# Optimization experiments

Measured on AMD Instinct MI355X. Metric: run time of the kernel, lower is better.

Reference implementation:

```python
import jax, jax.numpy as jnp
import numpy as np

N, E, F, H, C, G = 100000, 1600000, 128, 4, 32, 64
D = H * C  # 128, per-layer node dim
NEG_SLOPE = 0.2
BN_EPS = 1e-5


def setup_inputs() -> dict:
    key = jax.random.key(0)
    ks = jax.random.split(key, 24)
    inp = {
        "x": jax.random.normal(ks[0], (N, F), jnp.float32),
        "edge_index": jax.random.randint(ks[1], (2, E), 0, N, jnp.int64),
        "batch": jnp.sort(jax.random.randint(ks[2], (N,), 0, G, jnp.int64)),
        # GATConv layer 0: in=F, out=C per head
        "w0": jax.random.normal(ks[3], (F, H * C), jnp.float32) * 0.1,
        "att_src0": jax.random.normal(ks[4], (H, C), jnp.float32) * 0.1,
        "att_dst0": jax.random.normal(ks[5], (H, C), jnp.float32) * 0.1,
        "bias0": jax.random.normal(ks[6], (H * C,), jnp.float32) * 0.1,
        # GATConv layer 1: in=D, out=C per head
        "w1": jax.random.normal(ks[7], (D, H * C), jnp.float32) * 0.1,
        "att_src1": jax.random.normal(ks[8], (H, C), jnp.float32) * 0.1,
        "att_dst1": jax.random.normal(ks[9], (H, C), jnp.float32) * 0.1,
        "bias1": jax.random.normal(ks[10], (H * C,), jnp.float32) * 0.1,
        # BatchNorm (eval mode: running stats)
        "bn_g0": jax.random.normal(ks[11], (D,), jnp.float32) * 0.1 + 1.0,
        "bn_b0": jax.random.normal(ks[12], (D,), jnp.float32) * 0.1,
        "bn_m0": jax.random.normal(ks[13], (D,), jnp.float32) * 0.1,
        "bn_v0": jax.random.uniform(ks[14], (D,), jnp.float32) + 0.5,
        "bn_g1": jax.random.normal(ks[15], (D,), jnp.float32) * 0.1 + 1.0,
        "bn_b1": jax.random.normal(ks[16], (D,), jnp.float32) * 0.1,
        "bn_m1": jax.random.normal(ks[17], (D,), jnp.float32) * 0.1,
        "bn_v1": jax.random.uniform(ks[18], (D,), jnp.float32) + 0.5,
        # head MLP
        "lin1_w": jax.random.normal(ks[19], (D, D // 2), jnp.float32) * 0.1,
        "lin1_b": jax.random.normal(ks[20], (D // 2,), jnp.float32) * 0.1,
        "lin2_w": jax.random.normal(ks[21], (D // 2, 1), jnp.float32) * 0.1,
        "lin2_b": jax.random.normal(ks[22], (1,), jnp.float32) * 0.1,
    }
    return inp


def gat_conv(x, src, dst, w, att_s, att_d, bias):
    """PyG GATConv (concat=True, add_self_loops already in src/dst), eval mode."""
    n = x.shape[0]
    h = (x @ w).reshape(n, H, C)                       # [N,H,C]
    a_s = jnp.sum(h * att_s, axis=-1)                   # [N,H]
    a_d = jnp.sum(h * att_d, axis=-1)                   # [N,H]
    e = jax.nn.leaky_relu(a_s[src] + a_d[dst], NEG_SLOPE)  # [Etot,H]
    m = jax.ops.segment_max(e, dst, num_segments=n)
    m = jax.lax.stop_gradient(jnp.where(jnp.isfinite(m), m, 0.0))
    ex = jnp.exp(e - m[dst])
    denom = jax.ops.segment_sum(ex, dst, num_segments=n)
    alpha = ex / (denom[dst] + 1e-16)                    # segment softmax over dst
    out = jax.ops.segment_sum(h[src] * alpha[:, :, None], dst, num_segments=n)
    return out.reshape(n, H * C) + bias


def bn_eval(x, g, b, m, v):
    return (x - m) * jax.lax.rsqrt(v + BN_EPS) * g + b


def reference(x, edge_index, batch,
              w0, att_src0, att_dst0, bias0,
              w1, att_src1, att_dst1, bias1,
              bn_g0, bn_b0, bn_m0, bn_v0,
              bn_g1, bn_b1, bn_m1, bn_v1,
              lin1_w, lin1_b, lin2_w, lin2_b):
    n = x.shape[0]
    loops = jnp.arange(n, dtype=edge_index.dtype)
    src = jnp.concatenate([edge_index[0], loops])
    dst = jnp.concatenate([edge_index[1], loops])

    h = gat_conv(x, src, dst, w0, att_src0, att_dst0, bias0)
    h = jax.nn.relu(bn_eval(h, bn_g0, bn_b0, bn_m0, bn_v0))
    h = gat_conv(h, src, dst, w1, att_src1, att_dst1, bias1)
    h = jax.nn.relu(bn_eval(h, bn_g1, bn_b1, bn_m1, bn_v1))

    # global mean pool over graphs
    summed = jax.ops.segment_sum(h, batch, num_segments=G)           # [G,D]
    counts = jax.ops.segment_sum(jnp.ones((n,), h.dtype), batch, num_segments=G)
    pooled = summed / jnp.maximum(counts, 1.0)[:, None]

    z = jax.nn.relu(pooled @ lin1_w + lin1_b)
    return z @ lin2_w + lin2_b                                        # [G,1]
```

## Files before the change

### kernel.cpp

```cpp
#include <hip/hip_runtime.h>

#define GG 64
#define STRIDE 10240
#define NBINMAX 256

typedef __attribute__((ext_vector_type(8))) short short8;
typedef __attribute__((ext_vector_type(4))) float f32x4;


__device__ inline unsigned short bf16rne(float f) {
  unsigned int x = __float_as_uint(f);
  unsigned int r = (x + 0x7FFFu + ((x >> 16) & 1u)) >> 16;
  return (unsigned short)r;
}
__device__ inline unsigned int pack2(float a, float b) {
  return (unsigned int)bf16rne(a) | ((unsigned int)bf16rne(b) << 16);
}
__device__ inline float blo(unsigned int v) { return __uint_as_float(v << 16); }
__device__ inline float bhi(unsigned int v) { return __uint_as_float(v & 0xFFFF0000u); }


__global__ __launch_bounds__(256) void wprep(const float* __restrict__ w0,
                                             const float* __restrict__ w1,
                                             unsigned short* __restrict__ wt,
                                             int* __restrict__ gcur) {
  if (blockIdx.x == 0) gcur[threadIdx.x] = threadIdx.x * STRIDE;
  int idx = blockIdx.x * 256 + threadIdx.x;
  int layer = idx >> 14;
  int e = idx & 16383;
  int k = e >> 7, n = e & 127;
  float v = (layer ? w1 : w0)[e];
  unsigned short hi = bf16rne(v);
  float hif = __uint_as_float((unsigned int)hi << 16);
  unsigned short lo = bf16rne(v - hif);
  unsigned short* basep = wt + layer * 32768;
  basep[n * 128 + k] = hi;
  basep[16384 + n * 128 + k] = lo;
}


__global__ __launch_bounds__(512) void mega1(
    const float* __restrict__ in, const unsigned short* __restrict__ wtL,
    const float* __restrict__ att_s, const float* __restrict__ att_d,
    unsigned int* __restrict__ h16, float* __restrict__ a_s, float* __restrict__ a_d,
    const int* __restrict__ ei, int* __restrict__ gcur, unsigned int* __restrict__ pairs,
    const int* __restrict__ batch, int* __restrict__ gstart,
    int N, int E, int bG, int P1B) {
  __shared__ unsigned short xh[128][40], xl[128][40];
  __shared__ int hist[NBINMAX], gbase[NBINMAX], lcur[NBINMAX];
  int bid = blockIdx.x;
  int t = threadIdx.x;

  if (bid < bG) {
    int base = bid * 128;
    int lane = t & 63, w = t >> 6;
    int l15 = lane & 15, lg = lane >> 4;
    int hd = w & 3;
    int n0 = hd * 32;
    int rh = w >> 2;

    f32x4 zero4 = {0.f, 0.f, 0.f, 0.f};
    f32x4 acc[4][2];
    #pragma unroll
    for (int rt = 0; rt < 4; ++rt) { acc[rt][0] = zero4; acc[rt][1] = zero4; }

    int sr = t >> 2;
    int sc = (t & 3) * 8;
    int gr = base + sr;
    int rc = gr < N ? gr : (N - 1);
    const float* xpf = in + (size_t)rc * 128 + sc;

    const unsigned short* wh0 = &wtL[(size_t)(n0 + l15) * 128];
    const unsigned short* wh1 = &wtL[(size_t)(n0 + 16 + l15) * 128];

    float4 u0 = *(const float4*)(xpf + 0);
    float4 u1 = *(const float4*)(xpf + 4);
    short8 cbh0 = *(const short8*)(wh0 + lg * 8);
    short8 cbh1 = *(const short8*)(wh1 + lg * 8);
    short8 cbl0 = *(const short8*)(wh0 + 16384 + lg * 8);
    short8 cbl1 = *(const short8*)(wh1 + 16384 + lg * 8);

    #pragma unroll
    for (int kt = 0; kt < 4; ++kt) {
      if (kt) __syncthreads();
      {
        unsigned int b0 = __float_as_uint(u0.x), b1 = __float_as_uint(u0.y);
        unsigned int b2 = __float_as_uint(u0.z), b3 = __float_as_uint(u0.w);
        unsigned int b4 = __float_as_uint(u1.x), b5 = __float_as_uint(u1.y);
        unsigned int b6 = __float_as_uint(u1.z), b7 = __float_as_uint(u1.w);
        *(unsigned int*)&xh[sr][sc + 0] = __builtin_amdgcn_perm(b1, b0, 0x07060302u);
        *(unsigned int*)&xh[sr][sc + 2] = __builtin_amdgcn_perm(b3, b2, 0x07060302u);
        *(unsigned int*)&xh[sr][sc + 4] = __builtin_amdgcn_perm(b5, b4, 0x07060302u);
        *(unsigned int*)&xh[sr][sc + 6] = __builtin_amdgcn_perm(b7, b6, 0x07060302u);
        float r0 = u0.x - __uint_as_float(b0 & 0xFFFF0000u);
        float r1 = u0.y - __uint_as_float(b1 & 0xFFFF0000u);
        float r2 = u0.z - __uint_as_float(b2 & 0xFFFF0000u);
        float r3 = u0.w - __uint_as_float(b3 & 0xFFFF0000u);
        float r4 = u1.x - __uint_as_float(b4 & 0xFFFF0000u);
        float r5 = u1.y - __uint_as_float(b5 & 0xFFFF0000u);
        float r6 = u1.z - __uint_as_float(b6 & 0xFFFF0000u);
        float r7 = u1.w - __uint_as_float(b7 & 0xFFFF0000u);
        *(unsigned int*)&xl[sr][sc + 0] =
            __builtin_amdgcn_perm(__float_as_uint(r1), __float_as_uint(r0), 0x07060302u);
        *(unsigned int*)&xl[sr][sc + 2] =
            __builtin_amdgcn_perm(__float_as_uint(r3), __float_as_uint(r2), 0x07060302u);
        *(unsigned int*)&xl[sr][sc + 4] =
            __builtin_amdgcn_perm(__float_as_uint(r5), __float_as_uint(r4), 0x07060302u);
        *(unsigned int*)&xl[sr][sc + 6] =
            __builtin_amdgcn_perm(__float_as_uint(r7), __float_as_uint(r6), 0x07060302u);
      }
      __syncthreads();
      float4 v0 = u0, v1 = u1;
      short8 nbh0 = cbh0, nbh1 = cbh1, nbl0 = cbl0, nbl1 = cbl1;
      if (kt < 3) {
        int k1 = (kt + 1) * 32;
        v0 = *(const float4*)(xpf + k1);
        v1 = *(const float4*)(xpf + k1 + 4);
        nbh0 = *(const short8*)(wh0 + k1 + lg * 8);
        nbh1 = *(const short8*)(wh1 + k1 + lg * 8);
        nbl0 = *(const short8*)(wh0 + 16384 + k1 + lg * 8);
        nbl1 = *(const short8*)(wh1 + 16384 + k1 + lg * 8);
      }
      #pragma unroll
      for (int rt = 0; rt < 4; ++rt) {
        int row = rh * 64 + rt * 16 + l15;
        short8 fah = *(const short8*)&xh[row][lg * 8];
        short8 fal = *(const short8*)&xl[row][lg * 8];
        acc[rt][0] = __builtin_amdgcn_mfma_f32_16x16x32_bf16(fah, cbh0, acc[rt][0], 0, 0, 0);
        acc[rt][1] = __builtin_amdgcn_mfma_f32_16x16x32_bf16(fah, cbh1, acc[rt][1], 0, 0, 0);
        acc[rt][0] = __builtin_amdgcn_mfma_f32_16x16x32_bf16(fal, cbh0, acc[rt][0], 0, 0, 0);
        acc[rt][1] = __builtin_amdgcn_mfma_f32_16x16x32_bf16(fal, cbh1, acc[rt][1], 0, 0, 0);
        acc[rt][0] = __builtin_amdgcn_mfma_f32_16x16x32_bf16(fah, cbl0, acc[rt][0], 0, 0, 0);
        acc[rt][1] = __builtin_amdgcn_mfma_f32_16x16x32_bf16(fah, cbl1, acc[rt][1], 0, 0, 0);
      }
      u0 = v0; u1 = v1;
      cbh0 = nbh0; cbh1 = nbh1; cbl0 = nbl0; cbl1 = nbl1;
    }

    int headg = hd;
    float as0 = att_s[n0 + l15], as1 = att_s[n0 + 16 + l15];
    float ad0 = att_d[n0 + l15], ad1 = att_d[n0 + 16 + l15];
    #pragma unroll
    for (int rt = 0; rt < 4; ++rt) {
      float ps[4], pd[4];
      #pragma unroll
      for (int q = 0; q < 4; ++q) {
        float c0v = acc[rt][0][q], c1v = acc[rt][1][q];
        float pp0 = __shfl_xor(c0v, 1), pp1 = __shfl_xor(c1v, 1);
        int row = base + rh * 64 + rt * 16 + lg * 4 + q;
        if (!(l15 & 1) && row < N) {
          h16[(size_t)row * 64 + (n0 + l15) / 2]      = pack2(c0v, pp0);
          h16[(size_t)row * 64 + (n0 + 16 + l15) / 2] = pack2(c1v, pp1);
        }
        ps[q] = c0v * as0 + c1v * as1;
        pd[q] = c0v * ad0 + c1v * ad1;
      }
      #pragma unroll
      for (int m = 1; m <= 8; m <<= 1) {
        #pragma unroll
        for (int q = 0; q < 4; ++q) { ps[q] += __shfl_xor(ps[q], m); pd[q] += __shfl_xor(pd[q], m); }
      }
      if (l15 == 0) {
        #pragma unroll
        for (int q = 0; q < 4; ++q) {
          int row = base + rh * 64 + rt * 16 + lg * 4 + q;
          if (row < N) { a_s[row * 4 + headg] = ps[q]; a_d[row * 4 + headg] = pd[q]; }
        }
      }
    }
  } else if (bid < bG + P1B) {
    int tot = E + N;
    int base = (bid - bG) * 4096;
    if (t < NBINMAX) hist[t] = 0;
    __syncthreads();
    int sarr[8], darr[8];
    #pragma unroll
    for (int k = 0; k < 8; ++k) {
      int i = base + k * 512 + t;
      if (i < tot) {
        int s, d;
        if (i < E) { s = ei[i]; d = ei[E + i]; } else { s = i - E; d = s; }
        sarr[k] = s; darr[k] = d;
        atomicAdd(&hist[d >> 9], 1);
      } else darr[k] = -1;
    }
    __syncthreads();
    if (t < NBINMAX) {
      int c = hist[t];
      gbase[t] = (c > 0) ? atomicAdd(&gcur[t], c) : 0;
      lcur[t] = 0;
    }
    __syncthreads();
    #pragma unroll
    for (int k = 0; k < 8; ++k) {
      int d = darr[k];
      if (d >= 0) {
        int b = d >> 9;
        int p = gbase[b] + atomicAdd(&lcur[b], 1);
        pairs[p] = ((unsigned int)(d & 511) << 17) | (unsigned int)sarr[k];
      }
    }
  } else {
    int i = (bid - bG - P1B) * 512 + t;
    if (i < N) {
      int g = batch[i];
      if (i == 0 || batch[i - 1] != g) gstart[g] = i;
    }
  }
}


__global__ __launch_bounds__(256) void mega2(
    const unsigned int* __restrict__ pairs, const int* __restrict__ gcur,
    int* __restrict__ ssrc, int* __restrict__ offsets, int* __restrict__ counts,
    const int* __restrict__ gstart, int* __restrict__ go, int* __restrict__ ge,
    int N, int NBIN) {
  __shared__ int ncnt[512], ncur[512], excl_s[512];
  __shared__ int wsum[4];
  int b = blockIdx.x;
  int t = threadIdx.x;
  if (b < NBIN) {
    int pb = b * STRIDE;
    int cnt = gcur[b] - pb;
    ncnt[t] = 0; ncnt[t + 256] = 0;
    __syncthreads();
    for (int e = t; e < cnt; e += 256) {
      unsigned int v = pairs[pb + e];
      atomicAdd(&ncnt[v >> 17], 1);
    }
    __syncthreads();
    int c0 = ncnt[2 * t], c1 = ncnt[2 * t + 1];
    int ps = c0 + c1;
    int lane = t & 63, w = t >> 6;
    int x = ps;
    #pragma unroll
    for (int s = 1; s < 64; s <<= 1) { int y = __shfl_up(x, s); if (lane >= s) x += y; }
    if (lane == 63) wsum[w] = x;
    __syncthreads();
    int woff = 0;
    for (int i = 0; i < w; ++i) woff += wsum[i];
    int ep = woff + x - ps;
    excl_s[2 * t]     = ep;
    excl_s[2 * t + 1] = ep + c0;
    __syncthreads();
    int binstart = b << 9;
    for (int i = t; i < 512; i += 256) {
      ncur[i] = excl_s[i];
      int node = binstart + i;
      if (node < N) { offsets[node] = pb + excl_s[i]; counts[node] = ncnt[i]; }
    }
    __syncthreads();
    for (int e = t; e < cnt; e += 256) {
      unsigned int v = pairs[pb + e];
      int dl = v >> 17;
      int p = atomicAdd(&ncur[dl], 1);
      ssrc[pb + p] = (int)(v & 0x1FFFF);
    }
  } else if (t < 64) {
    int g = t;
    int s = gstart[g];
    int v = (s < 0) ? 0x7FFFFFFF : s;
    int suf = v;
    #pragma unroll
    for (int off = 1; off < 64; off <<= 1) {
      int x = __shfl_down(suf, off);
      if (g + off < 64) suf = min(suf, x);
    }
    int nxt = __shfl_down(suf, 1);
    if (g == 63) nxt = 0x7FFFFFFF;
    int e = nxt == 0x7FFFFFFF ? N : nxt;
    if (s < 0) { go[g] = e; ge[g] = e; }
    else       { go[g] = s; ge[g] = e; }
  }
}


__global__ __launch_bounds__(512) void gemm_bf16(
    const unsigned int* __restrict__ in, const unsigned short* __restrict__ wtL,
    const float* __restrict__ att_s, const float* __restrict__ att_d,
    unsigned int* __restrict__ h16, float* __restrict__ a_s,
    float* __restrict__ a_d, int N) {
  __shared__ unsigned short xh[128][40];
  int t = threadIdx.x;
  int base = blockIdx.x * 128;
  int lane = t & 63, w = t >> 6;
  int l15 = lane & 15, lg = lane >> 4;
  int hd = w & 3;
  int n0 = hd * 32;
  int rh = w >> 2;

  f32x4 zero4 = {0.f, 0.f, 0.f, 0.f};
  f32x4 acc[4][2];
  #pragma unroll
  for (int rt = 0; rt < 4; ++rt) { acc[rt][0] = zero4; acc[rt][1] = zero4; }

  int sr = t >> 2;
  int sc = (t & 3) * 8;
  int gr = base + sr;
  int rc = gr < N ? gr : (N - 1);
  const unsigned int* xpb = in + (size_t)rc * 64 + (sc >> 1);

  const unsigned short* wh0 = &wtL[(size_t)(n0 + l15) * 128];
  const unsigned short* wh1 = &wtL[(size_t)(n0 + 16 + l15) * 128];

  uint4 p0 = *(const uint4*)(xpb + 0);
  short8 cbh0 = *(const short8*)(wh0 + lg * 8);
  short8 cbh1 = *(const short8*)(wh1 + lg * 8);
  short8 cbl0 = *(const short8*)(wh0 + 16384 + lg * 8);
  short8 cbl1 = *(const short8*)(wh1 + 16384 + lg * 8);

  #pragma unroll
  for (int kt = 0; kt < 4; ++kt) {
    if (kt) __syncthreads();
    *(uint4*)&xh[sr][sc] = p0;
    __syncthreads();
    uint4 q0 = p0;
    short8 nbh0 = cbh0, nbh1 = cbh1, nbl0 = cbl0, nbl1 = cbl1;
    if (kt < 3) {
      int k1 = (kt + 1) * 32;
      q0 = *(const uint4*)(xpb + (k1 >> 1));
      nbh0 = *(const short8*)(wh0 + k1 + lg * 8);
      nbh1 = *(const short8*)(wh1 + k1 + lg * 8);
      nbl0 = *(const short8*)(wh0 + 16384 + k1 + lg * 8);
      nbl1 = *(const short8*)(wh1 + 16384 + k1 + lg * 8);
    }
    #pragma unroll
    for (int rt = 0; rt < 4; ++rt) {
      int row = rh * 64 + rt * 16 + l15;
      short8 fah = *(const short8*)&xh[row][lg * 8];
      acc[rt][0] = __builtin_amdgcn_mfma_f32_16x16x32_bf16(fah, cbh0, acc[rt][0], 0, 0, 0);
      acc[rt][1] = __builtin_amdgcn_mfma_f32_16x16x32_bf16(fah, cbh1, acc[rt][1], 0, 0, 0);
      acc[rt][0] = __builtin_amdgcn_mfma_f32_16x16x32_bf16(fah, cbl0, acc[rt][0], 0, 0, 0);
      acc[rt][1] = __builtin_amdgcn_mfma_f32_16x16x32_bf16(fah, cbl1, acc[rt][1], 0, 0, 0);
    }
    p0 = q0;
    cbh0 = nbh0; cbh1 = nbh1; cbl0 = nbl0; cbl1 = nbl1;
  }

  int headg = hd;
  float as0 = att_s[n0 + l15], as1 = att_s[n0 + 16 + l15];
  float ad0 = att_d[n0 + l15], ad1 = att_d[n0 + 16 + l15];
  #pragma unroll
  for (int rt = 0; rt < 4; ++rt) {
    float ps[4], pd[4];
    #pragma unroll
    for (int q = 0; q < 4; ++q) {
      float c0v = acc[rt][0][q], c1v = acc[rt][1][q];
      float pp0 = __shfl_xor(c0v, 1), pp1 = __shfl_xor(c1v, 1);
      int row = base + rh * 64 + rt * 16 + lg * 4 + q;
      if (!(l15 & 1) && row < N) {
        h16[(size_t)row * 64 + (n0 + l15) / 2]      = pack2(c0v, pp0);
        h16[(size_t)row * 64 + (n0 + 16 + l15) / 2] = pack2(c1v, pp1);
      }
      ps[q] = c0v * as0 + c1v * as1;
      pd[q] = c0v * ad0 + c1v * ad1;
    }
    #pragma unroll
    for (int m = 1; m <= 8; m <<= 1) {
      #pragma unroll
      for (int q = 0; q < 4; ++q) { ps[q] += __shfl_xor(ps[q], m); pd[q] += __shfl_xor(pd[q], m); }
    }
    if (l15 == 0) {
      #pragma unroll
      for (int q = 0; q < 4; ++q) {
        int row = base + rh * 64 + rt * 16 + lg * 4 + q;
        if (row < N) { a_s[row * 4 + headg] = ps[q]; a_d[row * 4 + headg] = pd[q]; }
      }
    }
  }
}


#define ACCP(EX, V0, V1)                                                       \
  { float2 ex2 = make_float2(EX, EX);                                          \
    acc2[0] += ex2 * make_float2(blo(V0.x), bhi(V0.x));                        \
    acc2[1] += ex2 * make_float2(blo(V0.y), bhi(V0.y));                        \
    acc2[2] += ex2 * make_float2(blo(V0.z), bhi(V0.z));                        \
    acc2[3] += ex2 * make_float2(blo(V0.w), bhi(V0.w));                        \
    acc2[4] += ex2 * make_float2(blo(V1.x), bhi(V1.x));                        \
    acc2[5] += ex2 * make_float2(blo(V1.y), bhi(V1.y));                        \
    acc2[6] += ex2 * make_float2(blo(V1.z), bhi(V1.z));                        \
    acc2[7] += ex2 * make_float2(blo(V1.w), bhi(V1.w)); }

__global__ __launch_bounds__(256) void gat_aggregate(
    const unsigned int* __restrict__ h16, const float* __restrict__ a_s, const float* __restrict__ a_d,
    const int* __restrict__ offsets, const int* __restrict__ counts, const int* __restrict__ ssrc,
    const float* __restrict__ bias,
    const float* __restrict__ bn_g, const float* __restrict__ bn_b,
    const float* __restrict__ bn_m, const float* __restrict__ bn_v,
    unsigned int* __restrict__ y16, int N) {
  __shared__ float part[4][8][132];
  int wv = threadIdx.x >> 6;
  int lane = threadIdx.x & 63;
  int wid = blockIdx.x * 4 + wv;
  if (wid >= N) return;
  int off = offsets[wid], cnt = counts[wid];
  int eg = lane >> 3;
  int j  = lane & 7;
  int hh = j >> 1;
  float ad = a_d[wid * 4 + hh];

  float2 acc2[8] = {};
  float den = 0.f;

  int sA = ssrc[off + (eg < cnt ? eg : 0)];
  int iB0 = eg + 8;
  int sB = ssrc[off + (iB0 < cnt ? iB0 : 0)];
  float asA = a_s[sA * 4 + hh];
  float asB = a_s[sB * 4 + hh];

  for (int i = eg; i < cnt; i += 16) {
    const uint4* hpA = (const uint4*)(h16 + (size_t)sA * 64 + j * 8);
    uint4 va0 = hpA[0], va1 = hpA[1];
    const uint4* hpB = (const uint4*)(h16 + (size_t)sB * 64 + j * 8);
    uint4 vb0 = hpB[0], vb1 = hpB[1];
    int in0 = i + 16, in1 = i + 24;
    int snA = ssrc[off + (in0 < cnt ? in0 : 0)];
    int snB = ssrc[off + (in1 < cnt ? in1 : 0)];
    float anA = a_s[snA * 4 + hh];
    float anB = a_s[snB * 4 + hh];
    float eA = asA + ad; eA = eA > 0.f ? eA : 0.2f * eA;
    float exA = __expf(eA);
    float eB = asB + ad; eB = eB > 0.f ? eB : 0.2f * eB;
    float exB = ((i + 8) < cnt) ? __expf(eB) : 0.f;
    den += exA + exB;
    ACCP(exA, va0, va1)
    ACCP(exB, vb0, vb1)
    sA = snA; sB = snB; asA = anA; asB = anB;
  }

  den += __shfl_xor(den, 8);
  den += __shfl_xor(den, 16);
  den += __shfl_xor(den, 32);
  den = __shfl(den, (lane >> 4) * 2);

  float* pw = &part[wv][eg][j * 16];
  *(float4*)(pw + 0)  = make_float4(acc2[0].x, acc2[0].y, acc2[1].x, acc2[1].y);
  *(float4*)(pw + 4)  = make_float4(acc2[2].x, acc2[2].y, acc2[3].x, acc2[3].y);
  *(float4*)(pw + 8)  = make_float4(acc2[4].x, acc2[4].y, acc2[5].x, acc2[5].y);
  *(float4*)(pw + 12) = make_float4(acc2[6].x, acc2[6].y, acc2[7].x, acc2[7].y);
  asm volatile("s_waitcnt lgkmcnt(0)" ::: "memory");

  int d = lane * 2;
  float r0 = 0.f, r1 = 0.f;
  #pragma unroll
  for (int g = 0; g < 8; ++g) {
    float2 v = *(const float2*)(&part[wv][g][d]);
    r0 += v.x; r1 += v.y;
  }

  float inv = 1.f / (den + 1e-16f);
  float2 bi = *(const float2*)(&bias[d]);
  float2 g2 = *(const float2*)(&bn_g[d]);
  float2 b2 = *(const float2*)(&bn_b[d]);
  float2 m2 = *(const float2*)(&bn_m[d]);
  float2 v2 = *(const float2*)(&bn_v[d]);
  float o0 = r0 * inv + bi.x;
  float o1 = r1 * inv + bi.y;
  o0 = fmaxf((o0 - m2.x) * (g2.x * rsqrtf(v2.x + 1e-5f)) + b2.x, 0.f);
  o1 = fmaxf((o1 - m2.y) * (g2.y * rsqrtf(v2.y + 1e-5f)) + b2.y, 0.f);
  y16[(size_t)wid * 64 + lane] = pack2(o0, o1);
}


#define POOLP 8

__global__ __launch_bounds__(256) void pool_kernel(const unsigned int* __restrict__ y16,
                                                   const int* __restrict__ go,
                                                   const int* __restrict__ ge,
                                                   float* __restrict__ pooled) {
  int g = blockIdx.x / POOLP, p = blockIdx.x % POOLP;
  int s = go[g], e = ge[g];
  int len = e - s;
  int q0 = s + (len * p) / POOLP, q1 = s + (len * (p + 1)) / POOLP;
  int t = threadIdx.x;
  int d = t & 127, half = t >> 7;
  int du = d >> 1, dodd = d & 1;
  float acc = 0.f;
  for (int i = q0 + half; i < q1; i += 2) {
    unsigned int v = y16[(size_t)i * 64 + du];
    acc += dodd ? bhi(v) : blo(v);
  }
  __shared__ float red[256];
  red[t] = acc;
  __syncthreads();
  if (half == 0) atomicAdd(&pooled[g * 128 + d], red[d] + red[d + 128]);
}

__global__ __launch_bounds__(64) void mlp_kernel(const float* __restrict__ pooled,
                                                 const int* __restrict__ go,
                                                 const int* __restrict__ ge,
                                                 const float* __restrict__ w1,
                                                 const float* __restrict__ b1,
                                                 const float* __restrict__ w2,
                                                 const float* __restrict__ b2,
                                                 float* __restrict__ out) {
  int g = blockIdx.x, j = threadIdx.x;
  int cnt = ge[g] - go[g];
  float inv = 1.f / (float)(cnt > 1 ? cnt : 1);
  float z = b1[j];
  for (int k = 0; k < 128; ++k) z += pooled[g * 128 + k] * inv * w1[k * 64 + j];
  z = fmaxf(z, 0.f);
  float v = z * w2[j];
  #pragma unroll
  for (int m = 1; m < 64; m <<= 1) v += __shfl_xor(v, m);
  if (j == 0) out[g] = v + b2[0];
}


extern "C" void kernel_launch(void* const* d_in, const int* in_sizes, int n_in,
                              void* d_out, int out_size, void* d_ws, size_t ws_size,
                              hipStream_t stream) {
  const float* x     = (const float*)d_in[0];
  const int*   ei    = (const int*)d_in[1];
  const int*   batch = (const int*)d_in[2];
  const float* w0    = (const float*)d_in[3];
  const float* atts0 = (const float*)d_in[4];
  const float* attd0 = (const float*)d_in[5];
  const float* bias0 = (const float*)d_in[6];
  const float* w1    = (const float*)d_in[7];
  const float* atts1 = (const float*)d_in[8];
  const float* attd1 = (const float*)d_in[9];
  const float* bias1 = (const float*)d_in[10];
  const float* bng0  = (const float*)d_in[11];
  const float* bnb0  = (const float*)d_in[12];
  const float* bnm0  = (const float*)d_in[13];
  const float* bnv0  = (const float*)d_in[14];
  const float* bng1  = (const float*)d_in[15];
  const float* bnb1  = (const float*)d_in[16];
  const float* bnm1  = (const float*)d_in[17];
  const float* bnv1  = (const float*)d_in[18];
  const float* l1w   = (const float*)d_in[19];
  const float* l1b   = (const float*)d_in[20];
  const float* l2w   = (const float*)d_in[21];
  const float* l2b   = (const float*)d_in[22];

  int N = in_sizes[2];
  int E = in_sizes[1] / 2;
  int tot = E + N;
  int NBIN = (N + 511) / 512;

  char* p = (char*)d_ws;
  unsigned int* h16 = (unsigned int*)p; p += (size_t)N * 64 * 4;
  unsigned int* y16 = (unsigned int*)p; p += (size_t)N * 64 * 4;
  float* a_s    = (float*)p; p += (size_t)N * 4 * 4;
  float* a_d    = (float*)p; p += (size_t)N * 4 * 4;
  int* counts   = (int*)p;   p += (size_t)N * 4;
  int* offsets  = (int*)p;   p += (size_t)N * 4;
  int* ssrc     = (int*)p;   p += (size_t)NBINMAX * STRIDE * 4;
  int* gcur     = (int*)p;   p += NBINMAX * 4;
  int* gstart   = (int*)p;   p += 64 * 4;
  int* go       = (int*)p;   p += 64 * 4;
  int* ge       = (int*)p;   p += 64 * 4;
  float* pooled = (float*)p; p += 64 * 128 * 4;
  unsigned short* wt = (unsigned short*)p; p += 2 * 32768 * 2;
  unsigned int* pairs = y16;

  hipMemsetAsync(gstart, 0xFF, 64 * 4, stream);
  hipMemsetAsync(pooled, 0, 64 * 128 * 4, stream);

  int bW = (N + 3) / 4;
  int bG = (N + 127) / 128;
  int P1B = (tot + 4095) / 4096;
  int BNB = (N + 511) / 512;

  wprep<<<128, 256, 0, stream>>>(w0, w1, wt, gcur);
  mega1<<<bG + P1B + BNB, 512, 0, stream>>>(x, wt, atts0, attd0, h16, a_s, a_d,
                                            ei, gcur, pairs, batch, gstart,
                                            N, E, bG, P1B);
  mega2<<<NBIN + 1, 256, 0, stream>>>(pairs, gcur, ssrc, offsets, counts,
                                      gstart, go, ge, N, NBIN);
  gat_aggregate<<<bW, 256, 0, stream>>>(h16, a_s, a_d, offsets, counts, ssrc,
                                        bias0, bng0, bnb0, bnm0, bnv0, y16, N);
  gemm_bf16<<<bG, 512, 0, stream>>>(y16, wt + 32768, atts1, attd1, h16, a_s, a_d, N);
  gat_aggregate<<<bW, 256, 0, stream>>>(h16, a_s, a_d, offsets, counts, ssrc,
                                        bias1, bng1, bnb1, bnm1, bnv1, y16, N);
  pool_kernel<<<GG * POOLP, 256, 0, stream>>>(y16, go, ge, pooled);
  mlp_kernel<<<GG, 64, 0, stream>>>(pooled, go, ge, l1w, l1b, l2w, l2b, (float*)d_out);
}
```

Baseline: 293.4 us.

## Process two destination nodes per wave in GAT aggregation and fold memsets into wprep

Result: faster. 284.1 us, median of 3 (-3.2%).

```diff
diff --git a/kernel.cpp b/kernel.cpp
--- a/kernel.cpp
+++ b/kernel.cpp
@@ -23,9 +23,14 @@
 __global__ __launch_bounds__(256) void wprep(const float* __restrict__ w0,
                                              const float* __restrict__ w1,
                                              unsigned short* __restrict__ wt,
-                                             int* __restrict__ gcur) {
-  if (blockIdx.x == 0) gcur[threadIdx.x] = threadIdx.x * STRIDE;
-  int idx = blockIdx.x * 256 + threadIdx.x;
+                                             int* __restrict__ gcur,
+                                             int* __restrict__ gstart,
+                                             float* __restrict__ pooled) {
+  int b = blockIdx.x, t = threadIdx.x;
+  if (b == 0) gcur[t] = t * STRIDE;
+  if (b == 1 && t < 64) gstart[t] = -1;
+  if (b >= 2 && b < 34) pooled[(b - 2) * 256 + t] = 0.f;
+  int idx = b * 256 + t;
   int layer = idx >> 14;
   int e = idx & 16383;
   int k = e >> 7, n = e & 127;
@@ -371,16 +376,16 @@
 }
 
 
-#define ACCP(EX, V0, V1)                                                       \
+#define ACCP(AC, EX, V0, V1)                                                   \
   { float2 ex2 = make_float2(EX, EX);                                          \
-    acc2[0] += ex2 * make_float2(blo(V0.x), bhi(V0.x));                        \
-    acc2[1] += ex2 * make_float2(blo(V0.y), bhi(V0.y));                        \
-    acc2[2] += ex2 * make_float2(blo(V0.z), bhi(V0.z));                        \
-    acc2[3] += ex2 * make_float2(blo(V0.w), bhi(V0.w));                        \
-    acc2[4] += ex2 * make_float2(blo(V1.x), bhi(V1.x));                        \
-    acc2[5] += ex2 * make_float2(blo(V1.y), bhi(V1.y));                        \
-    acc2[6] += ex2 * make_float2(blo(V1.z), bhi(V1.z));                        \
-    acc2[7] += ex2 * make_float2(blo(V1.w), bhi(V1.w)); }
+    AC[0] += ex2 * make_float2(blo(V0.x), bhi(V0.x));                          \
+    AC[1] += ex2 * make_float2(blo(V0.y), bhi(V0.y));                          \
+    AC[2] += ex2 * make_float2(blo(V0.z), bhi(V0.z));                          \
+    AC[3] += ex2 * make_float2(blo(V0.w), bhi(V0.w));                          \
+    AC[4] += ex2 * make_float2(blo(V1.x), bhi(V1.x));                          \
+    AC[5] += ex2 * make_float2(blo(V1.y), bhi(V1.y));                          \
+    AC[6] += ex2 * make_float2(blo(V1.z), bhi(V1.z));                          \
+    AC[7] += ex2 * make_float2(blo(V1.w), bhi(V1.w)); }
 
 __global__ __launch_bounds__(256) void gat_aggregate(
     const unsigned int* __restrict__ h16, const float* __restrict__ a_s, const float* __restrict__ a_d,
@@ -392,74 +397,167 @@
   __shared__ float part[4][8][132];
   int wv = threadIdx.x >> 6;
   int lane = threadIdx.x & 63;
-  int wid = blockIdx.x * 4 + wv;
-  if (wid >= N) return;
-  int off = offsets[wid], cnt = counts[wid];
+  int wid0 = blockIdx.x * 8 + wv * 2;
+  int wid1 = wid0 + 1;
+  if (wid0 >= N) return;
+  bool v1 = wid1 < N;
+  int w1c = v1 ? wid1 : 0;
   int eg = lane >> 3;
   int j  = lane & 7;
   int hh = j >> 1;
-  float ad = a_d[wid * 4 + hh];
-
-  float2 acc2[8] = {};
-  float den = 0.f;
-
-  int sA = ssrc[off + (eg < cnt ? eg : 0)];
-  int iB0 = eg + 8;
-  int sB = ssrc[off + (iB0 < cnt ? iB0 : 0)];
-  float asA = a_s[sA * 4 + hh];
-  float asB = a_s[sB * 4 + hh];
-
-  for (int i = eg; i < cnt; i += 16) {
-    const uint4* hpA = (const uint4*)(h16 + (size_t)sA * 64 + j * 8);
+
+  int off0 = offsets[wid0], cnt0 = counts[wid0];
+  int off1 = offsets[w1c],  cnt1 = v1 ? counts[w1c] : 0;
+  float ad0 = a_d[wid0 * 4 + hh];
+  float ad1 = a_d[w1c * 4 + hh];
+  int sA0 = ssrc[off0 + (eg < cnt0 ? eg : 0)];
+  int sB0 = ssrc[off0 + (eg + 8 < cnt0 ? eg + 8 : 0)];
+  int sA1 = ssrc[off1 + (eg < cnt1 ? eg : 0)];
+  int sB1 = ssrc[off1 + (eg + 8 < cnt1 ? eg + 8 : 0)];
+  float asA0 = a_s[sA0 * 4 + hh];
+  float asB0 = a_s[sB0 * 4 + hh];
+  float asA1 = a_s[sA1 * 4 + hh];
+  float asB1 = a_s[sB1 * 4 + hh];
+
+  float2 acc0[8] = {}, acc1[8] = {};
+  float den0 = 0.f, den1 = 0.f;
+
+  {
+    const uint4* hA0 = (const uint4*)(h16 + (size_t)sA0 * 64 + j * 8);
+    uint4 va0 = hA0[0], va1 = hA0[1];
+    const uint4* hB0 = (const uint4*)(h16 + (size_t)sB0 * 64 + j * 8);
+    uint4 vb0 = hB0[0], vb1 = hB0[1];
+    const uint4* hA1 = (const uint4*)(h16 + (size_t)sA1 * 64 + j * 8);
+    uint4 vc0 = hA1[0], vc1 = hA1[1];
+    const uint4* hB1 = (const uint4*)(h16 + (size_t)sB1 * 64 + j * 8);
+    uint4 vd0 = hB1[0], vd1 = hB1[1];
+    int n00 = 16 + eg, n01 = 24 + eg;
+    int t00 = ssrc[off0 + (n00 < cnt0 ? n00 : 0)];
+    int t01 = ssrc[off0 + (n01 < cnt0 ? n01 : 0)];
+    int t10 = ssrc[off1 + (n00 < cnt1 ? n00 : 0)];
+    int t11 = ssrc[off1 + (n01 < cnt1 ? n01 : 0)];
+    float u00 = a_s[t00 * 4 + hh];
+    float u01 = a_s[t01 * 4 + hh];
+    float u10 = a_s[t10 * 4 + hh];
+    float u11 = a_s[t11 * 4 + hh];
+    float e0 = asA0 + ad0; e0 = e0 > 0.f ? e0 : 0.2f * e0;
+    float e1 = asB0 + ad0; e1 = e1 > 0.f ? e1 : 0.2f * e1;
+    float x0 = (eg < cnt0)     ? __expf(e0) : 0.f;
+    float x1 = (eg + 8 < cnt0) ? __expf(e1) : 0.f;
+    den0 += x0 + x1;
+    ACCP(acc0, x0, va0, va1)
+    ACCP(acc0, x1, vb0, vb1)
+    float e2 = asA1 + ad1; e2 = e2 > 0.f ? e2 : 0.2f * e2;
+    float e3 = asB1 + ad1; e3 = e3 > 0.f ? e3 : 0.2f * e3;
+    float x2 = (eg < cnt1)     ? __expf(e2) : 0.f;
+    float x3 = (eg + 8 < cnt1) ? __expf(e3) : 0.f;
+    den1 += x2 + x3;
+    ACCP(acc1, x2, vc0, vc1)
+    ACCP(acc1, x3, vd0, vd1)
+    sA0 = t00; sB0 = t01; asA0 = u00; asB0 = u01;
+    sA1 = t10; sB1 = t11; asA1 = u10; asB1 = u11;
+  }
+
+  for (int i = eg + 16; i < cnt0; i += 16) {
+    const uint4* hpA = (const uint4*)(h16 + (size_t)sA0 * 64 + j * 8);
     uint4 va0 = hpA[0], va1 = hpA[1];
-    const uint4* hpB = (const uint4*)(h16 + (size_t)sB * 64 + j * 8);
+    const uint4* hpB = (const uint4*)(h16 + (size_t)sB0 * 64 + j * 8);
     uint4 vb0 = hpB[0], vb1 = hpB[1];
     int in0 = i + 16, in1 = i + 24;
-    int snA = ssrc[off + (in0 < cnt ? in0 : 0)];
-    int snB = ssrc[off + (in1 < cnt ? in1 : 0)];
+    int snA = ssrc[off0 + (in0 < cnt0 ? in0 : 0)];
+    int snB = ssrc[off0 + (in1 < cnt0 ? in1 : 0)];
     float anA = a_s[snA * 4 + hh];
     float anB = a_s[snB * 4 + hh];
-    float eA = asA + ad; eA = eA > 0.f ? eA : 0.2f * eA;
+    float eA = asA0 + ad0; eA = eA > 0.f ? eA : 0.2f * eA;
     float exA = __expf(eA);
-    float eB = asB + ad; eB = eB > 0.f ? eB : 0.2f * eB;
-    float exB = ((i + 8) < cnt) ? __expf(eB) : 0.f;
-    den += exA + exB;
-    ACCP(exA, va0, va1)
-    ACCP(exB, vb0, vb1)
-    sA = snA; sB = snB; asA = anA; asB = anB;
-  }
-
-  den += __shfl_xor(den, 8);
-  den += __shfl_xor(den, 16);
-  den += __shfl_xor(den, 32);
-  den = __shfl(den, (lane >> 4) * 2);
-
-  float* pw = &part[wv][eg][j * 16];
-  *(float4*)(pw + 0)  = make_float4(acc2[0].x, acc2[0].y, acc2[1].x, acc2[1].y);
-  *(float4*)(pw + 4)  = make_float4(acc2[2].x, acc2[2].y, acc2[3].x, acc2[3].y);
-  *(float4*)(pw + 8)  = make_float4(acc2[4].x, acc2[4].y, acc2[5].x, acc2[5].y);
-  *(float4*)(pw + 12) = make_float4(acc2[6].x, acc2[6].y, acc2[7].x, acc2[7].y);
-  asm volatile("s_waitcnt lgkmcnt(0)" ::: "memory");
+    float eB = asB0 + ad0; eB = eB > 0.f ? eB : 0.2f * eB;
+    float exB = ((i + 8) < cnt0) ? __expf(eB) : 0.f;
+    den0 += exA + exB;
+    ACCP(acc0, exA, va0, va1)
+    ACCP(acc0, exB, vb0, vb1)
+    sA0 = snA; sB0 = snB; asA0 = anA; asB0 = anB;
+  }
+  for (int i = eg + 16; i < cnt1; i += 16) {
+    const uint4* hpA = (const uint4*)(h16 + (size_t)sA1 * 64 + j * 8);
+    uint4 va0 = hpA[0], va1 = hpA[1];
+    const uint4* hpB = (const uint4*)(h16 + (size_t)sB1 * 64 + j * 8);
+    uint4 vb0 = hpB[0], vb1 = hpB[1];
+    int in0 = i + 16, in1 = i + 24;
+    int snA = ssrc[off1 + (in0 < cnt1 ? in0 : 0)];
+    int snB = ssrc[off1 + (in1 < cnt1 ? in1 : 0)];
+    float anA = a_s[snA * 4 + hh];
+    float anB = a_s[snB * 4 + hh];
+    float eA = asA1 + ad1; eA = eA > 0.f ? eA : 0.2f * eA;
+    float exA = __expf(eA);
+    float eB = asB1 + ad1; eB = eB > 0.f ? eB : 0.2f * eB;
+    float exB = ((i + 8) < cnt1) ? __expf(eB) : 0.f;
+    den1 += exA + exB;
+    ACCP(acc1, exA, va0, va1)
+    ACCP(acc1, exB, vb0, vb1)
+    sA1 = snA; sB1 = snB; asA1 = anA; asB1 = anB;
+  }
+
+  den0 += __shfl_xor(den0, 8);
+  den0 += __shfl_xor(den0, 16);
+  den0 += __shfl_xor(den0, 32);
+  den0 = __shfl(den0, (lane >> 4) * 2);
+  den1 += __shfl_xor(den1, 8);
+  den1 += __shfl_xor(den1, 16);
+  den1 += __shfl_xor(den1, 32);
+  den1 = __shfl(den1, (lane >> 4) * 2);
 
   int d = lane * 2;
-  float r0 = 0.f, r1 = 0.f;
-  #pragma unroll
-  for (int g = 0; g < 8; ++g) {
-    float2 v = *(const float2*)(&part[wv][g][d]);
-    r0 += v.x; r1 += v.y;
-  }
-
-  float inv = 1.f / (den + 1e-16f);
   float2 bi = *(const float2*)(&bias[d]);
   float2 g2 = *(const float2*)(&bn_g[d]);
   float2 b2 = *(const float2*)(&bn_b[d]);
   float2 m2 = *(const float2*)(&bn_m[d]);
   float2 v2 = *(const float2*)(&bn_v[d]);
-  float o0 = r0 * inv + bi.x;
-  float o1 = r1 * inv + bi.y;
-  o0 = fmaxf((o0 - m2.x) * (g2.x * rsqrtf(v2.x + 1e-5f)) + b2.x, 0.f);
-  o1 = fmaxf((o1 - m2.y) * (g2.y * rsqrtf(v2.y + 1e-5f)) + b2.y, 0.f);
-  y16[(size_t)wid * 64 + lane] = pack2(o0, o1);
+  float sc0 = g2.x * rsqrtf(v2.x + 1e-5f);
+  float sc1 = g2.y * rsqrtf(v2.y + 1e-5f);
+
+  float* pw = &part[wv][eg][j * 16];
+
+  *(float4*)(pw + 0)  = make_float4(acc0[0].x, acc0[0].y, acc0[1].x, acc0[1].y);
+  *(float4*)(pw + 4)  = make_float4(acc0[2].x, acc0[2].y, acc0[3].x, acc0[3].y);
+  *(float4*)(pw + 8)  = make_float4(acc0[4].x, acc0[4].y, acc0[5].x, acc0[5].y);
+  *(float4*)(pw + 12) = make_float4(acc0[6].x, acc0[6].y, acc0[7].x, acc0[7].y);
+  asm volatile("s_waitcnt lgkmcnt(0)" ::: "memory");
+  float r00 = 0.f, r01 = 0.f;
+  #pragma unroll
+  for (int g = 0; g < 8; ++g) {
+    float2 v = *(const float2*)(&part[wv][g][d]);
+    r00 += v.x; r01 += v.y;
+  }
+  asm volatile("s_waitcnt lgkmcnt(0)" ::: "memory");
+
+  *(float4*)(pw + 0)  = make_float4(acc1[0].x, acc1[0].y, acc1[1].x, acc1[1].y);
+  *(float4*)(pw + 4)  = make_float4(acc1[2].x, acc1[2].y, acc1[3].x, acc1[3].y);
+  *(float4*)(pw + 8)  = make_float4(acc1[4].x, acc1[4].y, acc1[5].x, acc1[5].y);
+  *(float4*)(pw + 12) = make_float4(acc1[6].x, acc1[6].y, acc1[7].x, acc1[7].y);
+  asm volatile("s_waitcnt lgkmcnt(0)" ::: "memory");
+  float r10 = 0.f, r11 = 0.f;
+  #pragma unroll
+  for (int g = 0; g < 8; ++g) {
+    float2 v = *(const float2*)(&part[wv][g][d]);
+    r10 += v.x; r11 += v.y;
+  }
+
+  {
+    float inv = 1.f / (den0 + 1e-16f);
+    float o0 = r00 * inv + bi.x;
+    float o1 = r01 * inv + bi.y;
+    o0 = fmaxf((o0 - m2.x) * sc0 + b2.x, 0.f);
+    o1 = fmaxf((o1 - m2.y) * sc1 + b2.y, 0.f);
+    y16[(size_t)wid0 * 64 + lane] = pack2(o0, o1);
+  }
+  if (v1) {
+    float inv = 1.f / (den1 + 1e-16f);
+    float o0 = r10 * inv + bi.x;
+    float o1 = r11 * inv + bi.y;
+    o0 = fmaxf((o0 - m2.x) * sc0 + b2.x, 0.f);
+    o1 = fmaxf((o1 - m2.y) * sc1 + b2.y, 0.f);
+    y16[(size_t)wid1 * 64 + lane] = pack2(o0, o1);
+  }
 }
 
 
@@ -556,25 +654,22 @@
   unsigned short* wt = (unsigned short*)p; p += 2 * 32768 * 2;
   unsigned int* pairs = y16;
 
-  hipMemsetAsync(gstart, 0xFF, 64 * 4, stream);
-  hipMemsetAsync(pooled, 0, 64 * 128 * 4, stream);
-
-  int bW = (N + 3) / 4;
+  int bW2 = (N + 7) / 8;
   int bG = (N + 127) / 128;
   int P1B = (tot + 4095) / 4096;
   int BNB = (N + 511) / 512;
 
-  wprep<<<128, 256, 0, stream>>>(w0, w1, wt, gcur);
+  wprep<<<128, 256, 0, stream>>>(w0, w1, wt, gcur, gstart, pooled);
   mega1<<<bG + P1B + BNB, 512, 0, stream>>>(x, wt, atts0, attd0, h16, a_s, a_d,
                                             ei, gcur, pairs, batch, gstart,
                                             N, E, bG, P1B);
   mega2<<<NBIN + 1, 256, 0, stream>>>(pairs, gcur, ssrc, offsets, counts,
                                       gstart, go, ge, N, NBIN);
-  gat_aggregate<<<bW, 256, 0, stream>>>(h16, a_s, a_d, offsets, counts, ssrc,
-                                        bias0, bng0, bnb0, bnm0, bnv0, y16, N);
+  gat_aggregate<<<bW2, 256, 0, stream>>>(h16, a_s, a_d, offsets, counts, ssrc,
+                                         bias0, bng0, bnb0, bnm0, bnv0, y16, N);
   gemm_bf16<<<bG, 512, 0, stream>>>(y16, wt + 32768, atts1, attd1, h16, a_s, a_d, N);
-  gat_aggregate<<<bW, 256, 0, stream>>>(h16, a_s, a_d, offsets, counts, ssrc,
-                                        bias1, bng1, bnb1, bnm1, bnv1, y16, N);
+  gat_aggregate<<<bW2, 256, 0, stream>>>(h16, a_s, a_d, offsets, counts, ssrc,
+                                         bias1, bng1, bnb1, bnm1, bnv1, y16, N);
   pool_kernel<<<GG * POOLP, 256, 0, stream>>>(y16, go, ge, pooled);
   mlp_kernel<<<GG, 64, 0, stream>>>(pooled, go, ge, l1w, l1b, l2w, l2b, (float*)d_out);
 }
```
